# Optimization experiments

Measured on AMD Instinct MI355X. Metric: run time of the kernel, lower is better.

The kernel has to match this reference:

```python
import math
import jax, jax.numpy as jnp
import numpy as np

EMB = 768
N_HEAD = 12
B, T = 8, 1024

def setup_inputs() -> dict:
    key = jax.random.key(0)
    ks = jax.random.split(key, 5)
    x = jax.random.normal(ks[0], (B, T, EMB), dtype=jnp.float32)
    # linear params (torch nn.Linear: y = x @ W.T + b); store as [in, out] for einsum
    s1 = 1.0 / math.sqrt(EMB)
    W_attn = jax.random.uniform(ks[1], (EMB, 3 * EMB), jnp.float32, -s1, s1)
    b_attn = jax.random.uniform(ks[2], (3 * EMB,), jnp.float32, -s1, s1)
    W_proj = jax.random.uniform(ks[3], (EMB, EMB), jnp.float32, -s1, s1)
    b_proj = jax.random.uniform(ks[4], (EMB,), jnp.float32, -s1, s1)
    return {"x": x, "W_attn": W_attn, "b_attn": b_attn, "W_proj": W_proj, "b_proj": b_proj}

def reference(x, W_attn, b_attn, W_proj, b_proj):
    Bb, Tt, C = x.shape
    hd = C // N_HEAD
    qkv = x @ W_attn + b_attn                       # [B,T,3C]
    q, k, v = jnp.split(qkv, 3, axis=-1)
    # [B,T,C] -> [B,H,T,hd]
    def to_heads(t):
        return t.reshape(Bb, Tt, N_HEAD, hd).transpose(0, 2, 1, 3)
    q, k, v = to_heads(q), to_heads(k), to_heads(v)
    scale = 1.0 / math.sqrt(hd)
    scores = jnp.einsum('bhqd,bhkd->bhqk', q, k) * scale   # [B,H,T,T]
    causal = jnp.tril(jnp.ones((Tt, Tt), dtype=bool))
    scores = jnp.where(causal[None, None], scores, jnp.float32(-jnp.inf))
    attn = jax.nn.softmax(scores, axis=-1)
    y = jnp.einsum('bhqk,bhkd->bhqd', attn, v)              # [B,H,T,hd]
    y = y.transpose(0, 2, 1, 3).reshape(Bb, Tt, C)
    return y @ W_proj + b_proj
```

## Files before the change

### kernel.cpp

```cpp
#include <hip/hip_runtime.h>
#include <hip/hip_bf16.h>

typedef __hip_bfloat16 bf16;
typedef __attribute__((ext_vector_type(8))) short  bfrag;
typedef __attribute__((ext_vector_type(4))) float  facc;
typedef __attribute__((ext_vector_type(4))) short  short4v;

#define B_   8
#define T_   1024
#define C_   768
#define H_   12
#define HD_  64
#define M_   (B_ * T_)
#define N3_  (3 * C_)

#define QSCALE_ 0.18033688011112042f
#define M2_     17.312340490667562f

__device__ __forceinline__ float fexp2(float x) { return __builtin_amdgcn_exp2f(x); }

__device__ __forceinline__ void gload_lds16(const bf16* g, bf16* l) {
    __builtin_amdgcn_global_load_lds((const __attribute__((address_space(1))) void*)g,
                                     (__attribute__((address_space(3))) void*)l, 16, 0, 0);
}
__device__ __forceinline__ short bfbits(float f) {
    bf16 b = __float2bfloat16(f);
    return *reinterpret_cast<short*>(&b);
}

#define XBLK 6144
#define WABLK 1728
__global__ __launch_bounds__(256) void cvt_all_kernel(
        const float* __restrict__ x,  bf16* __restrict__ xb,
        const float* __restrict__ wa, bf16* __restrict__ wat,
        const float* __restrict__ wp, bf16* __restrict__ wpt) {
    const int bid = blockIdx.x, t = threadIdx.x;
    if (bid < XBLK) {
        const size_t i = ((size_t)bid * 256 + t) * 4;
        const float4 v = *(const float4*)(x + i);
        bf16* o = xb + i;
        o[0] = __float2bfloat16(v.x); o[1] = __float2bfloat16(v.y);
        o[2] = __float2bfloat16(v.z); o[3] = __float2bfloat16(v.w);
        return;
    }
    __shared__ float tile[32][33];
    const float* w; bf16* wt; int N, tI;
    if (bid < XBLK + WABLK) { w = wa; wt = wat; N = N3_; tI = bid - XBLK; }
    else                    { w = wp; wt = wpt; N = C_;  tI = bid - XBLK - WABLK; }
    const int ntn = N / 32;
    const int n0 = (tI % ntn) * 32, k0 = (tI / ntn) * 32;
    const int tx = t & 31, ty = t >> 5;
    for (int i = ty; i < 32; i += 8) tile[i][tx] = w[(size_t)(k0 + i) * N + n0 + tx];
    __syncthreads();
    for (int i = ty; i < 32; i += 8)
        wt[(size_t)(n0 + i) * C_ + k0 + tx] = __float2bfloat16(tile[tx][i]);
}


template<bool SWAPPED>
__device__ __forceinline__ void gemm_db_core(
        const bf16* __restrict__ Ap, const bf16* __restrict__ Bp,
        const int m0, const int n0, bf16* smem, facc (&acc)[4][6]) {
    constexpr int KD = 768, NT = 12;
    bf16* As = smem;
    bf16* Bs = smem + 2 * 8192;
    const int t = threadIdx.x, w = t >> 6, lane = t & 63;
    const int wrow = (w >> 1) * 64;
    const int wcol = (w & 1) * 96;
    const int fr = lane & 15, quad = lane >> 4;
    const int pc0 = (quad ^ (fr & 7)) * 8;
    const int pc1 = ((quad + 4) ^ (fr & 7)) * 8;
    const int srow = t >> 3;
    const int schunk = ((t & 7) ^ (srow & 7)) * 8;
    const int sdo = t * 8;

    const bf16* Ag = Ap + (size_t)(m0 + srow) * KD + schunk;
    const bf16* Bg = Bp + (size_t)(n0 + srow) * KD + schunk;

#pragma unroll
    for (int i = 0; i < 4; ++i)
#pragma unroll
        for (int c = 0; c < 6; ++c)
#pragma unroll
            for (int r = 0; r < 4; ++r) acc[i][c][r] = 0.f;

    auto stageA = [&](bf16* dst, int k0) {
        const bf16* s = Ag + k0;
        bf16* d = dst + sdo;
#pragma unroll
        for (int r = 0; r < 4; ++r)
            gload_lds16(s + (size_t)(r * 32) * KD, d + r * 2048);
    };
    auto stageB = [&](bf16* dst, int k0) {
        const bf16* s = Bg + k0;
        bf16* d = dst + sdo;
#pragma unroll
        for (int r = 0; r < 6; ++r)
            gload_lds16(s + (size_t)(r * 32) * KD, d + r * 2048);
    };

    stageA(As, 0);
    stageB(Bs, 0);
    __syncthreads();

#pragma unroll 2
    for (int kt = 0; kt < NT; ++kt) {
        const int cb = kt & 1;
        const bf16* AsC = As + cb * 8192;
        const bf16* BsC = Bs + cb * 12288;
        if (kt + 1 < NT) {
            stageA(As + (cb ^ 1) * 8192,  (kt + 1) * 64);
            stageB(Bs + (cb ^ 1) * 12288, (kt + 1) * 64);
        }
        bfrag af[4][2];
#pragma unroll
        for (int i = 0; i < 4; ++i) {
            const bf16* ar = AsC + (wrow + i * 16 + fr) * 64;
            af[i][0] = *(const bfrag*)(ar + pc0);
            af[i][1] = *(const bfrag*)(ar + pc1);
        }
#pragma unroll
        for (int c = 0; c < 6; ++c) {
            const bf16* br = BsC + (wcol + c * 16 + fr) * 64;
            bfrag b0 = *(const bfrag*)(br + pc0);
            bfrag b1 = *(const bfrag*)(br + pc1);
#pragma unroll
            for (int i = 0; i < 4; ++i) {
                if constexpr (SWAPPED) {
                    acc[i][c] = __builtin_amdgcn_mfma_f32_16x16x32_bf16(b0, af[i][0], acc[i][c], 0, 0, 0);
                    acc[i][c] = __builtin_amdgcn_mfma_f32_16x16x32_bf16(b1, af[i][1], acc[i][c], 0, 0, 0);
                } else {
                    acc[i][c] = __builtin_amdgcn_mfma_f32_16x16x32_bf16(af[i][0], b0, acc[i][c], 0, 0, 0);
                    acc[i][c] = __builtin_amdgcn_mfma_f32_16x16x32_bf16(af[i][1], b1, acc[i][c], 0, 0, 0);
                }
            }
        }
        __syncthreads();
    }
}

__global__ __launch_bounds__(256, 2) void qkv_db_kernel(
        const bf16* __restrict__ xb, const bf16* __restrict__ wat,
        const float* __restrict__ bias,
        bf16* __restrict__ Q, bf16* __restrict__ K, bf16* __restrict__ Vt) {
    extern __shared__ bf16 smem[];
    const int id = blockIdx.x;
    const int wg = (id & 7) * 96 + (id >> 3);
    const int bx = wg % 12, by = wg / 12;
    const int m0 = by * 128, n0 = bx * 192;
    const int which = n0 / C_;

    facc acc[4][6];
    if (which < 2) gemm_db_core<true >(xb, wat, m0, n0, smem, acc);
    else           gemm_db_core<false>(xb, wat, m0, n0, smem, acc);

    const int t = threadIdx.x, w = t >> 6, lane = t & 63;
    const int wr = (w >> 1) * 64, wc = (w & 1) * 96;
    const int fr = lane & 15, quad = lane >> 4;
    const int bb = m0 >> 10;
    if (which < 2) {
        bf16* dst = which ? K : Q;
        const float sc = which ? 1.0f : QSCALE_;
#pragma unroll
        for (int i = 0; i < 4; ++i) {
            const int tt = (m0 & 1023) + wr + i * 16 + fr;
#pragma unroll
            for (int c = 0; c < 6; ++c) {
                const int colbase = n0 + wc + c * 16 + quad * 4;
                const int cc = colbase - which * C_;
                const int h = cc >> 6, d0 = cc & 63;
                const float4 bv = *(const float4*)(bias + colbase);
                short4v pk;
                pk[0] = bfbits((acc[i][c][0] + bv.x) * sc);
                pk[1] = bfbits((acc[i][c][1] + bv.y) * sc);
                pk[2] = bfbits((acc[i][c][2] + bv.z) * sc);
                pk[3] = bfbits((acc[i][c][3] + bv.w) * sc);
                *(short4v*)(dst + ((size_t)(bb * H_ + h) * T_ + tt) * HD_ + d0) = pk;
            }
        }
    } else {
#pragma unroll
        for (int i = 0; i < 4; ++i) {
            const int tt0 = (m0 & 1023) + wr + i * 16 + quad * 4;
#pragma unroll
            for (int c = 0; c < 6; ++c) {
                const int col = n0 + wc + c * 16 + fr;
                const int cc = col - 2 * C_;
                const int h = cc >> 6, d = cc & 63;
                const float bv = bias[col];
                short4v pk;
                pk[0] = bfbits(acc[i][c][0] + bv);
                pk[1] = bfbits(acc[i][c][1] + bv);
                pk[2] = bfbits(acc[i][c][2] + bv);
                pk[3] = bfbits(acc[i][c][3] + bv);
                *(short4v*)(Vt + ((size_t)(bb * H_ + h) * HD_ + d) * T_ + tt0) = pk;
            }
        }
    }
}

__global__ __launch_bounds__(256, 2) void proj_db_kernel(
        const bf16* __restrict__ y, const bf16* __restrict__ wpt,
        const float* __restrict__ bias, float* __restrict__ out) {
    extern __shared__ bf16 smem[];
    const int id = blockIdx.x;
    const int wg = (id & 7) * 32 + (id >> 3);
    const int bx = wg % 4, by = wg / 4;
    const int m0 = by * 128, n0 = bx * 192;

    facc acc[4][6];
    gemm_db_core<true>(y, wpt, m0, n0, smem, acc);

    const int t = threadIdx.x, w = t >> 6, lane = t & 63;
    const int wr = (w >> 1) * 64, wc = (w & 1) * 96;
    const int fr = lane & 15, quad = lane >> 4;
#pragma unroll
    for (int i = 0; i < 4; ++i) {
        const int row = m0 + wr + i * 16 + fr;
#pragma unroll
        for (int c = 0; c < 6; ++c) {
            const int colbase = n0 + wc + c * 16 + quad * 4;
            const float4 bv = *(const float4*)(bias + colbase);
            float4 v;
            v.x = acc[i][c][0] + bv.x;
            v.y = acc[i][c][1] + bv.y;
            v.z = acc[i][c][2] + bv.z;
            v.w = acc[i][c][3] + bv.w;
            *(float4*)(out + (size_t)row * C_ + colbase) = v;
        }
    }
}

__global__ __launch_bounds__(256) void flash_attn_kernel(
        const bf16* __restrict__ Q, const bf16* __restrict__ K,
        const bf16* __restrict__ Vt, bf16* __restrict__ Y) {
    const int id   = blockIdx.x;
    const int bh   = (id & 7) * 12 + ((id >> 3) % 12);
    const int qpair = (id >> 3) / 12;
    const int t = threadIdx.x, w = t >> 6, lane = t & 63;
    const int fr = lane & 15, quad = lane >> 4, fq = quad * 8;

    __shared__ bf16 sK[2][64 * 64];
    __shared__ bf16 sVt[2][64 * 64];
    __shared__ bf16 sP[4][16][72];

    const bf16* Kbh = K  + (size_t)bh * T_ * HD_;
    const bf16* Vbh = Vt + (size_t)bh * HD_ * T_;
    const int b_ = bh / H_, h_ = bh % H_;

    const int srow = t >> 3;
    const int sgc  = ((t & 7) ^ (srow & 7)) * 8;
    const int c0   = (quad ^ (fr & 7)) * 8;

    for (int phase = 0; phase < 2; ++phase) {
        const int qt = (phase == 0) ? (15 - qpair) : qpair;
        const int q0 = qt * 64;

        const bf16* qbase = Q + ((size_t)bh * T_ + q0 + w * 16 + fr) * HD_;
        bfrag qa0 = *(const bfrag*)(qbase + fq);
        bfrag qa1 = *(const bfrag*)(qbase + 32 + fq);

        facc o[4];
        for (int nb = 0; nb < 4; ++nb) for (int r = 0; r < 4; ++r) o[nb][r] = 0.f;
        float rowl[4] = {0.f, 0.f, 0.f, 0.f};

        auto tile_step = [&](int kt, const bf16* sKp, const bf16* sVp) {
            const int k0 = kt * 64;
            facc s[4];
            for (int nb = 0; nb < 4; ++nb) for (int r = 0; r < 4; ++r) s[nb][r] = 0.f;
            for (int nb = 0; nb < 4; ++nb) {
                const bf16* kr = sKp + (nb * 16 + fr) * 64;
                bfrag kb0 = *(const bfrag*)(kr + c0);
                bfrag kb1 = *(const bfrag*)(kr + (c0 ^ 32));
                s[nb] = __builtin_amdgcn_mfma_f32_16x16x32_bf16(qa0, kb0, s[nb], 0, 0, 0);
                s[nb] = __builtin_amdgcn_mfma_f32_16x16x32_bf16(qa1, kb1, s[nb], 0, 0, 0);
            }
            const int mrow0 = q0 + w * 16 + quad * 4;
            float p[4][4];
            if (kt == qt) {
                for (int nb = 0; nb < 4; ++nb) {
                    const int n_g = k0 + nb * 16 + fr;
                    for (int r = 0; r < 4; ++r) {
                        const float a = (n_g > mrow0 + r) ? -1e30f : s[nb][r] - M2_;
                        p[nb][r] = fexp2(a);
                    }
                }
            } else {
                for (int nb = 0; nb < 4; ++nb)
                    for (int r = 0; r < 4; ++r)
                        p[nb][r] = fexp2(s[nb][r] - M2_);
            }
            for (int r = 0; r < 4; ++r)
                rowl[r] += p[0][r] + p[1][r] + p[2][r] + p[3][r];
            for (int nb = 0; nb < 4; ++nb)
                for (int r = 0; r < 4; ++r)
                    sP[w][quad * 4 + r][nb * 16 + fr] = __float2bfloat16(p[nb][r]);
            bfrag pa0 = *(const bfrag*)(&sP[w][fr][fq]);
            bfrag pa1 = *(const bfrag*)(&sP[w][fr][32 + fq]);
            for (int nb = 0; nb < 4; ++nb) {
                const bf16* vr = sVp + (nb * 16 + fr) * 64;
                bfrag vb0 = *(const bfrag*)(vr + c0);
                bfrag vb1 = *(const bfrag*)(vr + (c0 ^ 32));
                o[nb] = __builtin_amdgcn_mfma_f32_16x16x32_bf16(pa0, vb0, o[nb], 0, 0, 0);
                o[nb] = __builtin_amdgcn_mfma_f32_16x16x32_bf16(pa1, vb1, o[nb], 0, 0, 0);
            }
        };

        for (int kt = 0; kt <= qt; kt += 2) {
            const int k0 = kt * 64;
            const bool two = (kt + 1 <= qt);
            gload_lds16(Kbh + (size_t)(k0 + srow) * HD_ + sgc,      sK[0] + t * 8);
            gload_lds16(Kbh + (size_t)(k0 + 32 + srow) * HD_ + sgc, sK[0] + 2048 + t * 8);
            gload_lds16(Vbh + (size_t)srow * T_ + k0 + sgc,         sVt[0] + t * 8);
            gload_lds16(Vbh + (size_t)(srow + 32) * T_ + k0 + sgc,  sVt[0] + 2048 + t * 8);
            if (two) {
                const int k1 = k0 + 64;
                gload_lds16(Kbh + (size_t)(k1 + srow) * HD_ + sgc,      sK[1] + t * 8);
                gload_lds16(Kbh + (size_t)(k1 + 32 + srow) * HD_ + sgc, sK[1] + 2048 + t * 8);
                gload_lds16(Vbh + (size_t)srow * T_ + k1 + sgc,         sVt[1] + t * 8);
                gload_lds16(Vbh + (size_t)(srow + 32) * T_ + k1 + sgc,  sVt[1] + 2048 + t * 8);
            }
            __syncthreads();
            tile_step(kt, sK[0], sVt[0]);
            if (two) tile_step(kt + 1, sK[1], sVt[1]);
            __syncthreads();
        }

        for (int r = 0; r < 4; ++r) {
            float l = rowl[r];
            l += __shfl_xor(l, 1);
            l += __shfl_xor(l, 2);
            l += __shfl_xor(l, 4);
            l += __shfl_xor(l, 8);
            const float inv = 1.0f / l;
            const int tt = q0 + w * 16 + quad * 4 + r;
            bf16* yrow = Y + ((size_t)b_ * T_ + tt) * C_ + h_ * HD_;
            for (int nb = 0; nb < 4; ++nb)
                yrow[nb * 16 + fr] = __float2bfloat16(o[nb][r] * inv);
        }
    }
}

extern "C" void kernel_launch(void* const* d_in, const int* in_sizes, int n_in,
                              void* d_out, int out_size, void* d_ws, size_t ws_size,
                              hipStream_t stream) {
    const float* x      = (const float*)d_in[0];
    const float* W_attn = (const float*)d_in[1];
    const float* b_attn = (const float*)d_in[2];
    const float* W_proj = (const float*)d_in[3];
    const float* b_proj = (const float*)d_in[4];
    float* out = (float*)d_out;

    const size_t per = (size_t)B_ * H_ * T_ * HD_;
    bf16* Q   = (bf16*)d_ws;
    bf16* K   = Q + per;
    bf16* Vt  = K + per;
    bf16* XbY = Vt + per;
    bf16* WaT = XbY + per;
    bf16* WpT = WaT + (size_t)N3_ * C_;

    static bool s_attr = false;
    if (!s_attr) {
        hipFuncSetAttribute((const void*)qkv_db_kernel,
                            hipFuncAttributeMaxDynamicSharedMemorySize, 81920);
        hipFuncSetAttribute((const void*)proj_db_kernel,
                            hipFuncAttributeMaxDynamicSharedMemorySize, 81920);
        s_attr = true;
    }

    cvt_all_kernel<<<dim3(XBLK + WABLK + 576), dim3(256), 0, stream>>>(
        x, XbY, W_attn, WaT, W_proj, WpT);
    qkv_db_kernel<<<dim3(768), dim3(256), 81920, stream>>>(
        XbY, WaT, b_attn, Q, K, Vt);
    flash_attn_kernel<<<dim3(768), dim3(256), 0, stream>>>(Q, K, Vt, XbY);
    proj_db_kernel<<<dim3(256), dim3(256), 81920, stream>>>(
        XbY, WpT, b_proj, out);
}
```

Baseline: 175.8 us.

## Halve GEMM N-tile to 96, stagger K start per block, prioritize attention MFMA

The QKV and projection GEMMs switch from 128x192 to 128x96 tiles, which doubles the block count (1536 and 512) and cuts LDS per block so more blocks fit per CU. Each block also starts its K loop at a rotated offset, spreading concurrent blocks across different K slices to reduce contention on the same global lines. The attention kernel raises wave priority around its MFMA sections with s_setprio. Smaller tiles lower per-block operand reuse and add extra A-tile traffic.

```diff
diff --git a/kernel.cpp b/kernel.cpp
--- a/kernel.cpp
+++ b/kernel.cpp
@@ -58,15 +58,16 @@
 
 
 template<bool SWAPPED>
-__device__ __forceinline__ void gemm_db_core(
+__device__ __forceinline__ void gemm96_core(
         const bf16* __restrict__ Ap, const bf16* __restrict__ Bp,
-        const int m0, const int n0, bf16* smem, facc (&acc)[4][6]) {
+        const int m0, const int n0, const int kt0,
+        bf16* smem, facc (&acc)[4][3]) {
     constexpr int KD = 768, NT = 12;
     bf16* As = smem;
     bf16* Bs = smem + 2 * 8192;
     const int t = threadIdx.x, w = t >> 6, lane = t & 63;
     const int wrow = (w >> 1) * 64;
-    const int wcol = (w & 1) * 96;
+    const int wcol = (w & 1) * 48;
     const int fr = lane & 15, quad = lane >> 4;
     const int pc0 = (quad ^ (fr & 7)) * 8;
     const int pc1 = ((quad + 4) ^ (fr & 7)) * 8;
@@ -80,7 +81,7 @@
 #pragma unroll
     for (int i = 0; i < 4; ++i)
 #pragma unroll
-        for (int c = 0; c < 6; ++c)
+        for (int c = 0; c < 3; ++c)
 #pragma unroll
             for (int r = 0; r < 4; ++r) acc[i][c][r] = 0.f;
 
@@ -95,22 +96,24 @@
         const bf16* s = Bg + k0;
         bf16* d = dst + sdo;
 #pragma unroll
-        for (int r = 0; r < 6; ++r)
+        for (int r = 0; r < 3; ++r)
             gload_lds16(s + (size_t)(r * 32) * KD, d + r * 2048);
     };
 
-    stageA(As, 0);
-    stageB(Bs, 0);
+    stageA(As, kt0 * 64);
+    stageB(Bs, kt0 * 64);
     __syncthreads();
 
+    int kt = kt0;
 #pragma unroll 2
-    for (int kt = 0; kt < NT; ++kt) {
-        const int cb = kt & 1;
+    for (int s = 0; s < NT; ++s) {
+        const int cb = s & 1;
         const bf16* AsC = As + cb * 8192;
-        const bf16* BsC = Bs + cb * 12288;
-        if (kt + 1 < NT) {
-            stageA(As + (cb ^ 1) * 8192,  (kt + 1) * 64);
-            stageB(Bs + (cb ^ 1) * 12288, (kt + 1) * 64);
+        const bf16* BsC = Bs + cb * 6144;
+        const int ktn = (kt + 1 == NT) ? 0 : kt + 1;
+        if (s + 1 < NT) {
+            stageA(As + (cb ^ 1) * 8192, ktn * 64);
+            stageB(Bs + (cb ^ 1) * 6144, ktn * 64);
         }
         bfrag af[4][2];
 #pragma unroll
@@ -120,7 +123,7 @@
             af[i][1] = *(const bfrag*)(ar + pc1);
         }
 #pragma unroll
-        for (int c = 0; c < 6; ++c) {
+        for (int c = 0; c < 3; ++c) {
             const bf16* br = BsC + (wcol + c * 16 + fr) * 64;
             bfrag b0 = *(const bfrag*)(br + pc0);
             bfrag b1 = *(const bfrag*)(br + pc1);
@@ -136,26 +139,28 @@
             }
         }
         __syncthreads();
-    }
-}
-
-__global__ __launch_bounds__(256, 2) void qkv_db_kernel(
+        kt = ktn;
+    }
+}
+
+__global__ __launch_bounds__(256, 2) void qkv_s_kernel(
         const bf16* __restrict__ xb, const bf16* __restrict__ wat,
         const float* __restrict__ bias,
         bf16* __restrict__ Q, bf16* __restrict__ K, bf16* __restrict__ Vt) {
     extern __shared__ bf16 smem[];
     const int id = blockIdx.x;
-    const int wg = (id & 7) * 96 + (id >> 3);
-    const int bx = wg % 12, by = wg / 12;
-    const int m0 = by * 128, n0 = bx * 192;
+    const int wg = (id & 7) * 192 + (id >> 3);
+    const int bx = wg % 24, by = wg / 24;
+    const int m0 = by * 128, n0 = bx * 96;
+    const int kt0 = (id >> 3) % 12;
     const int which = n0 / C_;
 
-    facc acc[4][6];
-    if (which < 2) gemm_db_core<true >(xb, wat, m0, n0, smem, acc);
-    else           gemm_db_core<false>(xb, wat, m0, n0, smem, acc);
+    facc acc[4][3];
+    if (which < 2) gemm96_core<true >(xb, wat, m0, n0, kt0, smem, acc);
+    else           gemm96_core<false>(xb, wat, m0, n0, kt0, smem, acc);
 
     const int t = threadIdx.x, w = t >> 6, lane = t & 63;
-    const int wr = (w >> 1) * 64, wc = (w & 1) * 96;
+    const int wr = (w >> 1) * 64, wc = (w & 1) * 48;
     const int fr = lane & 15, quad = lane >> 4;
     const int bb = m0 >> 10;
     if (which < 2) {
@@ -165,7 +170,7 @@
         for (int i = 0; i < 4; ++i) {
             const int tt = (m0 & 1023) + wr + i * 16 + fr;
 #pragma unroll
-            for (int c = 0; c < 6; ++c) {
+            for (int c = 0; c < 3; ++c) {
                 const int colbase = n0 + wc + c * 16 + quad * 4;
                 const int cc = colbase - which * C_;
                 const int h = cc >> 6, d0 = cc & 63;
@@ -183,7 +188,7 @@
         for (int i = 0; i < 4; ++i) {
             const int tt0 = (m0 & 1023) + wr + i * 16 + quad * 4;
 #pragma unroll
-            for (int c = 0; c < 6; ++c) {
+            for (int c = 0; c < 3; ++c) {
                 const int col = n0 + wc + c * 16 + fr;
                 const int cc = col - 2 * C_;
                 const int h = cc >> 6, d = cc & 63;
@@ -199,26 +204,27 @@
     }
 }
 
-__global__ __launch_bounds__(256, 2) void proj_db_kernel(
+__global__ __launch_bounds__(256, 2) void proj_s_kernel(
         const bf16* __restrict__ y, const bf16* __restrict__ wpt,
         const float* __restrict__ bias, float* __restrict__ out) {
     extern __shared__ bf16 smem[];
     const int id = blockIdx.x;
-    const int wg = (id & 7) * 32 + (id >> 3);
-    const int bx = wg % 4, by = wg / 4;
-    const int m0 = by * 128, n0 = bx * 192;
-
-    facc acc[4][6];
-    gemm_db_core<true>(y, wpt, m0, n0, smem, acc);
+    const int wg = (id & 7) * 64 + (id >> 3);
+    const int bx = wg % 8, by = wg / 8;
+    const int m0 = by * 128, n0 = bx * 96;
+    const int kt0 = (id >> 3) % 12;
+
+    facc acc[4][3];
+    gemm96_core<true>(y, wpt, m0, n0, kt0, smem, acc);
 
     const int t = threadIdx.x, w = t >> 6, lane = t & 63;
-    const int wr = (w >> 1) * 64, wc = (w & 1) * 96;
+    const int wr = (w >> 1) * 64, wc = (w & 1) * 48;
     const int fr = lane & 15, quad = lane >> 4;
 #pragma unroll
     for (int i = 0; i < 4; ++i) {
         const int row = m0 + wr + i * 16 + fr;
 #pragma unroll
-        for (int c = 0; c < 6; ++c) {
+        for (int c = 0; c < 3; ++c) {
             const int colbase = n0 + wc + c * 16 + quad * 4;
             const float4 bv = *(const float4*)(bias + colbase);
             float4 v;
@@ -268,6 +274,7 @@
             const int k0 = kt * 64;
             facc s[4];
             for (int nb = 0; nb < 4; ++nb) for (int r = 0; r < 4; ++r) s[nb][r] = 0.f;
+            __builtin_amdgcn_s_setprio(1);
             for (int nb = 0; nb < 4; ++nb) {
                 const bf16* kr = sKp + (nb * 16 + fr) * 64;
                 bfrag kb0 = *(const bfrag*)(kr + c0);
@@ -275,6 +282,7 @@
                 s[nb] = __builtin_amdgcn_mfma_f32_16x16x32_bf16(qa0, kb0, s[nb], 0, 0, 0);
                 s[nb] = __builtin_amdgcn_mfma_f32_16x16x32_bf16(qa1, kb1, s[nb], 0, 0, 0);
             }
+            __builtin_amdgcn_s_setprio(0);
             const int mrow0 = q0 + w * 16 + quad * 4;
             float p[4][4];
             if (kt == qt) {
@@ -297,6 +305,7 @@
                     sP[w][quad * 4 + r][nb * 16 + fr] = __float2bfloat16(p[nb][r]);
             bfrag pa0 = *(const bfrag*)(&sP[w][fr][fq]);
             bfrag pa1 = *(const bfrag*)(&sP[w][fr][32 + fq]);
+            __builtin_amdgcn_s_setprio(1);
             for (int nb = 0; nb < 4; ++nb) {
                 const bf16* vr = sVp + (nb * 16 + fr) * 64;
                 bfrag vb0 = *(const bfrag*)(vr + c0);
@@ -304,6 +313,7 @@
                 o[nb] = __builtin_amdgcn_mfma_f32_16x16x32_bf16(pa0, vb0, o[nb], 0, 0, 0);
                 o[nb] = __builtin_amdgcn_mfma_f32_16x16x32_bf16(pa1, vb1, o[nb], 0, 0, 0);
             }
+            __builtin_amdgcn_s_setprio(0);
         };
 
         for (int kt = 0; kt <= qt; kt += 2) {
@@ -361,18 +371,18 @@
 
     static bool s_attr = false;
     if (!s_attr) {
-        hipFuncSetAttribute((const void*)qkv_db_kernel,
-                            hipFuncAttributeMaxDynamicSharedMemorySize, 81920);
-        hipFuncSetAttribute((const void*)proj_db_kernel,
-                            hipFuncAttributeMaxDynamicSharedMemorySize, 81920);
+        hipFuncSetAttribute((const void*)qkv_s_kernel,
+                            hipFuncAttributeMaxDynamicSharedMemorySize, 57344);
+        hipFuncSetAttribute((const void*)proj_s_kernel,
+                            hipFuncAttributeMaxDynamicSharedMemorySize, 57344);
         s_attr = true;
     }
 
     cvt_all_kernel<<<dim3(XBLK + WABLK + 576), dim3(256), 0, stream>>>(
         x, XbY, W_attn, WaT, W_proj, WpT);
-    qkv_db_kernel<<<dim3(768), dim3(256), 81920, stream>>>(
+    qkv_s_kernel<<<dim3(1536), dim3(256), 57344, stream>>>(
         XbY, WaT, b_attn, Q, K, Vt);
     flash_attn_kernel<<<dim3(768), dim3(256), 0, stream>>>(Q, K, Vt, XbY);
-    proj_db_kernel<<<dim3(256), dim3(256), 81920, stream>>>(
+    proj_s_kernel<<<dim3(512), dim3(256), 57344, stream>>>(
         XbY, WpT, b_proj, out);
 }
```

Result: no change. 176.4 us (+0.3%).

## Pre-pack GEMM operands into MFMA fragment layout and load directly from global

Applied to the files above, without the earlier changes.

The conversion kernel now writes x and both weight matrices in a fragment-packed bf16 layout. Each 16x32 MFMA fragment is stored contiguously, so every lane reads its 8 elements with one 16-byte global load. The QKV and projection GEMMs drop LDS staging, double buffering and barriers, read fragments straight from global memory and cache, and raise occupancy to 3 waves per SIMD. The attention kernel writes its output through LDS in the same packed layout and adds s_setprio around its MFMA blocks. The risk is that the GEMMs lose LDS reuse and latency hiding, leaving them exposed to global and L2 load latency.

```diff
diff --git a/kernel.cpp b/kernel.cpp
--- a/kernel.cpp
+++ b/kernel.cpp
@@ -13,6 +13,7 @@
 #define HD_  64
 #define M_   (B_ * T_)
 #define N3_  (3 * C_)
+#define NFK_ 24
 
 #define QSCALE_ 0.18033688011112042f
 #define M2_     17.312340490667562f
@@ -28,55 +29,53 @@
     return *reinterpret_cast<short*>(&b);
 }
 
-#define XBLK 6144
-#define WABLK 1728
-__global__ __launch_bounds__(256) void cvt_all_kernel(
-        const float* __restrict__ x,  bf16* __restrict__ xb,
-        const float* __restrict__ wa, bf16* __restrict__ wat,
-        const float* __restrict__ wp, bf16* __restrict__ wpt) {
+
+#define XPK 3072
+#define WAPK 1728
+__global__ __launch_bounds__(256) void cvt_pk_kernel(
+        const float* __restrict__ x,  bf16* __restrict__ xpk,
+        const float* __restrict__ wa, bf16* __restrict__ wapk,
+        const float* __restrict__ wp, bf16* __restrict__ wppk) {
     const int bid = blockIdx.x, t = threadIdx.x;
-    if (bid < XBLK) {
-        const size_t i = ((size_t)bid * 256 + t) * 4;
-        const float4 v = *(const float4*)(x + i);
-        bf16* o = xb + i;
-        o[0] = __float2bfloat16(v.x); o[1] = __float2bfloat16(v.y);
-        o[2] = __float2bfloat16(v.z); o[3] = __float2bfloat16(v.w);
+    if (bid < XPK) {
+        const int lane = t & 63;
+        const int gfrag = bid * 4 + (t >> 6);
+        const int row = (gfrag / NFK_) * 16 + (lane & 15);
+        const int col = (gfrag % NFK_) * 32 + (lane >> 4) * 8;
+        const float4 v0 = *(const float4*)(x + (size_t)row * C_ + col);
+        const float4 v1 = *(const float4*)(x + (size_t)row * C_ + col + 4);
+        bfrag v;
+        v[0] = bfbits(v0.x); v[1] = bfbits(v0.y); v[2] = bfbits(v0.z); v[3] = bfbits(v0.w);
+        v[4] = bfbits(v1.x); v[5] = bfbits(v1.y); v[6] = bfbits(v1.z); v[7] = bfbits(v1.w);
+        *(bfrag*)((unsigned short*)xpk + (size_t)gfrag * 512 + lane * 8) = v;
         return;
     }
     __shared__ float tile[32][33];
     const float* w; bf16* wt; int N, tI;
-    if (bid < XBLK + WABLK) { w = wa; wt = wat; N = N3_; tI = bid - XBLK; }
-    else                    { w = wp; wt = wpt; N = C_;  tI = bid - XBLK - WABLK; }
+    if (bid < XPK + WAPK) { w = wa; wt = wapk; N = N3_; tI = bid - XPK; }
+    else                  { w = wp; wt = wppk; N = C_;  tI = bid - XPK - WAPK; }
     const int ntn = N / 32;
     const int n0 = (tI % ntn) * 32, k0 = (tI / ntn) * 32;
     const int tx = t & 31, ty = t >> 5;
     for (int i = ty; i < 32; i += 8) tile[i][tx] = w[(size_t)(k0 + i) * N + n0 + tx];
     __syncthreads();
-    for (int i = ty; i < 32; i += 8)
-        wt[(size_t)(n0 + i) * C_ + k0 + tx] = __float2bfloat16(tile[tx][i]);
-}
-
+    if (t < 128) {
+        const int f = t >> 6, l = t & 63;
+        const int nl = f * 16 + (l & 15), k8 = (l >> 4) * 8;
+        bfrag v;
+#pragma unroll
+        for (int j = 0; j < 8; ++j) v[j] = bfbits(tile[k8 + j][nl]);
+        const size_t fid = (size_t)(n0 / 16 + f) * NFK_ + (k0 / 32);
+        *(bfrag*)((unsigned short*)wt + fid * 512 + (size_t)l * 8) = v;
+    }
+}
 
 template<bool SWAPPED>
-__device__ __forceinline__ void gemm_db_core(
-        const bf16* __restrict__ Ap, const bf16* __restrict__ Bp,
-        const int m0, const int n0, bf16* smem, facc (&acc)[4][6]) {
-    constexpr int KD = 768, NT = 12;
-    bf16* As = smem;
-    bf16* Bs = smem + 2 * 8192;
-    const int t = threadIdx.x, w = t >> 6, lane = t & 63;
-    const int wrow = (w >> 1) * 64;
-    const int wcol = (w & 1) * 96;
-    const int fr = lane & 15, quad = lane >> 4;
-    const int pc0 = (quad ^ (fr & 7)) * 8;
-    const int pc1 = ((quad + 4) ^ (fr & 7)) * 8;
-    const int srow = t >> 3;
-    const int schunk = ((t & 7) ^ (srow & 7)) * 8;
-    const int sdo = t * 8;
-
-    const bf16* Ag = Ap + (size_t)(m0 + srow) * KD + schunk;
-    const bf16* Bg = Bp + (size_t)(n0 + srow) * KD + schunk;
-
+__device__ __forceinline__ void gemm_pk_core(
+        const unsigned short* __restrict__ Ap0, const unsigned short* __restrict__ Bp0,
+        const int rtA, const int rtB, const int lane, facc (&acc)[4][6]) {
+    const unsigned short* Ap = Ap0 + (size_t)rtA * NFK_ * 512 + lane * 8;
+    const unsigned short* Bp = Bp0 + (size_t)rtB * NFK_ * 512 + lane * 8;
 #pragma unroll
     for (int i = 0; i < 4; ++i)
 #pragma unroll
@@ -84,78 +83,55 @@
 #pragma unroll
             for (int r = 0; r < 4; ++r) acc[i][c][r] = 0.f;
 
-    auto stageA = [&](bf16* dst, int k0) {
-        const bf16* s = Ag + k0;
-        bf16* d = dst + sdo;
-#pragma unroll
-        for (int r = 0; r < 4; ++r)
-            gload_lds16(s + (size_t)(r * 32) * KD, d + r * 2048);
-    };
-    auto stageB = [&](bf16* dst, int k0) {
-        const bf16* s = Bg + k0;
-        bf16* d = dst + sdo;
-#pragma unroll
-        for (int r = 0; r < 6; ++r)
-            gload_lds16(s + (size_t)(r * 32) * KD, d + r * 2048);
-    };
-
-    stageA(As, 0);
-    stageB(Bs, 0);
-    __syncthreads();
-
-#pragma unroll 2
-    for (int kt = 0; kt < NT; ++kt) {
-        const int cb = kt & 1;
-        const bf16* AsC = As + cb * 8192;
-        const bf16* BsC = Bs + cb * 12288;
-        if (kt + 1 < NT) {
-            stageA(As + (cb ^ 1) * 8192,  (kt + 1) * 64);
-            stageB(Bs + (cb ^ 1) * 12288, (kt + 1) * 64);
-        }
+    for (int kc = 0; kc < NFK_; kc += 2) {
         bfrag af[4][2];
 #pragma unroll
         for (int i = 0; i < 4; ++i) {
-            const bf16* ar = AsC + (wrow + i * 16 + fr) * 64;
-            af[i][0] = *(const bfrag*)(ar + pc0);
-            af[i][1] = *(const bfrag*)(ar + pc1);
+            af[i][0] = *(const bfrag*)(Ap + (size_t)(i * NFK_ + kc) * 512);
+            af[i][1] = *(const bfrag*)(Ap + (size_t)(i * NFK_ + kc + 1) * 512);
         }
 #pragma unroll
         for (int c = 0; c < 6; ++c) {
-            const bf16* br = BsC + (wcol + c * 16 + fr) * 64;
-            bfrag b0 = *(const bfrag*)(br + pc0);
-            bfrag b1 = *(const bfrag*)(br + pc1);
+            const bfrag b0 = *(const bfrag*)(Bp + (size_t)(c * NFK_ + kc) * 512);
+            const bfrag b1 = *(const bfrag*)(Bp + (size_t)(c * NFK_ + kc + 1) * 512);
 #pragma unroll
             for (int i = 0; i < 4; ++i) {
-                if constexpr (SWAPPED) {
+                if constexpr (SWAPPED)
                     acc[i][c] = __builtin_amdgcn_mfma_f32_16x16x32_bf16(b0, af[i][0], acc[i][c], 0, 0, 0);
+                else
+                    acc[i][c] = __builtin_amdgcn_mfma_f32_16x16x32_bf16(af[i][0], b0, acc[i][c], 0, 0, 0);
+            }
+#pragma unroll
+            for (int i = 0; i < 4; ++i) {
+                if constexpr (SWAPPED)
                     acc[i][c] = __builtin_amdgcn_mfma_f32_16x16x32_bf16(b1, af[i][1], acc[i][c], 0, 0, 0);
-                } else {
-                    acc[i][c] = __builtin_amdgcn_mfma_f32_16x16x32_bf16(af[i][0], b0, acc[i][c], 0, 0, 0);
+                else
                     acc[i][c] = __builtin_amdgcn_mfma_f32_16x16x32_bf16(af[i][1], b1, acc[i][c], 0, 0, 0);
-                }
-            }
-        }
-        __syncthreads();
-    }
-}
-
-__global__ __launch_bounds__(256, 2) void qkv_db_kernel(
-        const bf16* __restrict__ xb, const bf16* __restrict__ wat,
+            }
+        }
+    }
+}
+
+__global__ __launch_bounds__(256, 3) void qkv_pk_kernel(
+        const bf16* __restrict__ xpk, const bf16* __restrict__ wapk,
         const float* __restrict__ bias,
         bf16* __restrict__ Q, bf16* __restrict__ K, bf16* __restrict__ Vt) {
-    extern __shared__ bf16 smem[];
     const int id = blockIdx.x;
-    const int wg = (id & 7) * 96 + (id >> 3);
-    const int bx = wg % 12, by = wg / 12;
+    const int xcd = id & 7, L = id >> 3;
+    const int rgrp = xcd >> 1, cgrp = xcd & 1;
+    const int r_l = L & 15, c_l = L >> 4;
+    const int by = rgrp * 16 + r_l, bx = cgrp * 6 + c_l;
     const int m0 = by * 128, n0 = bx * 192;
-    const int which = n0 / C_;
-
-    facc acc[4][6];
-    if (which < 2) gemm_db_core<true >(xb, wat, m0, n0, smem, acc);
-    else           gemm_db_core<false>(xb, wat, m0, n0, smem, acc);
+    const int which = bx / 4;
 
     const int t = threadIdx.x, w = t >> 6, lane = t & 63;
     const int wr = (w >> 1) * 64, wc = (w & 1) * 96;
+    const int rtA = (m0 + wr) >> 4, rtB = (n0 + wc) >> 4;
+
+    facc acc[4][6];
+    if (which < 2) gemm_pk_core<true >((const unsigned short*)xpk, (const unsigned short*)wapk, rtA, rtB, lane, acc);
+    else           gemm_pk_core<false>((const unsigned short*)xpk, (const unsigned short*)wapk, rtA, rtB, lane, acc);
+
     const int fr = lane & 15, quad = lane >> 4;
     const int bb = m0 >> 10;
     if (which < 2) {
@@ -199,20 +175,21 @@
     }
 }
 
-__global__ __launch_bounds__(256, 2) void proj_db_kernel(
-        const bf16* __restrict__ y, const bf16* __restrict__ wpt,
+__global__ __launch_bounds__(256, 3) void proj_pk_kernel(
+        const bf16* __restrict__ ypk, const bf16* __restrict__ wppk,
         const float* __restrict__ bias, float* __restrict__ out) {
-    extern __shared__ bf16 smem[];
     const int id = blockIdx.x;
     const int wg = (id & 7) * 32 + (id >> 3);
-    const int bx = wg % 4, by = wg / 4;
+    const int bx = wg & 3, by = wg >> 2;
     const int m0 = by * 128, n0 = bx * 192;
-
-    facc acc[4][6];
-    gemm_db_core<true>(y, wpt, m0, n0, smem, acc);
 
     const int t = threadIdx.x, w = t >> 6, lane = t & 63;
     const int wr = (w >> 1) * 64, wc = (w & 1) * 96;
+    const int rtA = (m0 + wr) >> 4, rtB = (n0 + wc) >> 4;
+
+    facc acc[4][6];
+    gemm_pk_core<true>((const unsigned short*)ypk, (const unsigned short*)wppk, rtA, rtB, lane, acc);
+
     const int fr = lane & 15, quad = lane >> 4;
 #pragma unroll
     for (int i = 0; i < 4; ++i) {
@@ -268,6 +245,7 @@
             const int k0 = kt * 64;
             facc s[4];
             for (int nb = 0; nb < 4; ++nb) for (int r = 0; r < 4; ++r) s[nb][r] = 0.f;
+            __builtin_amdgcn_s_setprio(1);
             for (int nb = 0; nb < 4; ++nb) {
                 const bf16* kr = sKp + (nb * 16 + fr) * 64;
                 bfrag kb0 = *(const bfrag*)(kr + c0);
@@ -275,6 +253,7 @@
                 s[nb] = __builtin_amdgcn_mfma_f32_16x16x32_bf16(qa0, kb0, s[nb], 0, 0, 0);
                 s[nb] = __builtin_amdgcn_mfma_f32_16x16x32_bf16(qa1, kb1, s[nb], 0, 0, 0);
             }
+            __builtin_amdgcn_s_setprio(0);
             const int mrow0 = q0 + w * 16 + quad * 4;
             float p[4][4];
             if (kt == qt) {
@@ -297,6 +276,7 @@
                     sP[w][quad * 4 + r][nb * 16 + fr] = __float2bfloat16(p[nb][r]);
             bfrag pa0 = *(const bfrag*)(&sP[w][fr][fq]);
             bfrag pa1 = *(const bfrag*)(&sP[w][fr][32 + fq]);
+            __builtin_amdgcn_s_setprio(1);
             for (int nb = 0; nb < 4; ++nb) {
                 const bf16* vr = sVp + (nb * 16 + fr) * 64;
                 bfrag vb0 = *(const bfrag*)(vr + c0);
@@ -304,6 +284,7 @@
                 o[nb] = __builtin_amdgcn_mfma_f32_16x16x32_bf16(pa0, vb0, o[nb], 0, 0, 0);
                 o[nb] = __builtin_amdgcn_mfma_f32_16x16x32_bf16(pa1, vb1, o[nb], 0, 0, 0);
             }
+            __builtin_amdgcn_s_setprio(0);
         };
 
         for (int kt = 0; kt <= qt; kt += 2) {
@@ -326,17 +307,25 @@
             __syncthreads();
         }
 
+        float invr[4];
         for (int r = 0; r < 4; ++r) {
             float l = rowl[r];
             l += __shfl_xor(l, 1);
             l += __shfl_xor(l, 2);
             l += __shfl_xor(l, 4);
             l += __shfl_xor(l, 8);
-            const float inv = 1.0f / l;
-            const int tt = q0 + w * 16 + quad * 4 + r;
-            bf16* yrow = Y + ((size_t)b_ * T_ + tt) * C_ + h_ * HD_;
-            for (int nb = 0; nb < 4; ++nb)
-                yrow[nb * 16 + fr] = __float2bfloat16(o[nb][r] * inv);
+            invr[r] = 1.0f / l;
+        }
+        for (int nb = 0; nb < 4; ++nb)
+            for (int r = 0; r < 4; ++r)
+                sP[w][quad * 4 + r][nb * 16 + fr] = __float2bfloat16(o[nb][r] * invr[r]);
+        const int mt = (b_ * T_ + q0 + w * 16) >> 4;
+        unsigned short* Yp = (unsigned short*)Y;
+#pragma unroll
+        for (int kk2 = 0; kk2 < 2; ++kk2) {
+            const int kc = h_ * 2 + kk2;
+            bfrag v = *(const bfrag*)(&sP[w][lane & 15][kk2 * 32 + (lane >> 4) * 8]);
+            *(bfrag*)(Yp + (size_t)(mt * NFK_ + kc) * 512 + (size_t)lane * 8) = v;
         }
     }
 }
@@ -359,20 +348,11 @@
     bf16* WaT = XbY + per;
     bf16* WpT = WaT + (size_t)N3_ * C_;
 
-    static bool s_attr = false;
-    if (!s_attr) {
-        hipFuncSetAttribute((const void*)qkv_db_kernel,
-                            hipFuncAttributeMaxDynamicSharedMemorySize, 81920);
-        hipFuncSetAttribute((const void*)proj_db_kernel,
-                            hipFuncAttributeMaxDynamicSharedMemorySize, 81920);
-        s_attr = true;
-    }
-
-    cvt_all_kernel<<<dim3(XBLK + WABLK + 576), dim3(256), 0, stream>>>(
+    cvt_pk_kernel<<<dim3(XPK + WAPK + 576), dim3(256), 0, stream>>>(
         x, XbY, W_attn, WaT, W_proj, WpT);
-    qkv_db_kernel<<<dim3(768), dim3(256), 81920, stream>>>(
+    qkv_pk_kernel<<<dim3(768), dim3(256), 0, stream>>>(
         XbY, WaT, b_attn, Q, K, Vt);
     flash_attn_kernel<<<dim3(768), dim3(256), 0, stream>>>(Q, K, Vt, XbY);
-    proj_db_kernel<<<dim3(256), dim3(256), 81920, stream>>>(
+    proj_pk_kernel<<<dim3(256), dim3(256), 0, stream>>>(
         XbY, WpT, b_proj, out);
 }
```

Measured after the change: 216.9 us. 1.23x slower.
